# Performance work log

Measured on AMD Instinct MI355X. Metric: run time of the kernel, lower is better.

## Reference

```python
import jax, jax.numpy as jnp
import numpy as np

D_M, D_K, D_V, HEADS = 1024, 64, 64, 16
B, S = 2, 2048


def setup_inputs() -> dict:
    key = jax.random.key(0)
    ks = jax.random.split(key, 5)
    x = jax.random.normal(ks[0], (B, S, D_M), dtype=jnp.float32)
    # per-head projection weights (original deep-copies one rand init per head;
    # we give each head independent weights, matching the per-head param structure)
    Wk = jax.random.uniform(ks[1], (HEADS, D_M, D_K), dtype=jnp.float32)
    Wq = jax.random.uniform(ks[2], (HEADS, D_M, D_K), dtype=jnp.float32)
    Wv = jax.random.uniform(ks[3], (HEADS, D_M, D_V), dtype=jnp.float32)
    Wo = jax.random.uniform(ks[4], (HEADS * D_V, D_M), dtype=jnp.float32)
    return {"x": x, "Wk": Wk, "Wq": Wq, "Wv": Wv, "Wo": Wo}


def reference(x, Wk, Wq, Wv, Wo):
    # per-head QKV projections, batched over heads: [B,H,S,d]
    q = jnp.einsum("bsm,hmk->bhsk", x, Wq)
    k = jnp.einsum("bsm,hmk->bhsk", x, Wk)
    v = jnp.einsum("bsm,hmv->bhsv", x, Wv)
    scale = 1.0 / jnp.sqrt(jnp.asarray(q.shape[-1], dtype=q.dtype))
    scores = jnp.einsum("bhsk,bhtk->bhst", q, k) * scale  # [B,H,S,S]
    attn = jax.nn.softmax(scores, axis=-1)
    ctx = jnp.einsum("bhst,bhtv->bhsv", attn, v)  # [B,H,S,d_v]
    # concat heads -> [B,S,H*d_v], then output projection
    ctx = jnp.transpose(ctx, (0, 2, 1, 3)).reshape(x.shape[0], x.shape[1], -1)
    return jnp.einsum("bsc,cm->bsm", ctx, Wo)
```

## Files before the change

### kernel.cpp

```cpp
#include <hip/hip_runtime.h>
#include <hip/hip_bf16.h>
#include <stdint.h>

#define DM   1024
#define DKV  64
#define HEADS 16
#define BATCH 2
#define SEQ  2048
#define BS   (BATCH*SEQ)
#define BHD  (BATCH*HEADS)

typedef __attribute__((ext_vector_type(8))) short bf16x8;
typedef __attribute__((ext_vector_type(4))) short bf16x4;
typedef __attribute__((ext_vector_type(4))) float f32x4;

__device__ inline unsigned fb(float f) { union { float f; unsigned u; } v; v.f = f; return v.u; }

__device__ inline unsigned short bf16_rtn(float f) {
  unsigned u = fb(f);
  unsigned r = u + 0x7fffu + ((u >> 16) & 1u);
  return (unsigned short)(r >> 16);
}
__device__ inline float bf16_to_f(unsigned short h) {
  union { unsigned u; float f; } v; v.u = ((unsigned)h) << 16; return v.f;
}
__device__ inline void split_bf16(float x, unsigned short& hi, unsigned short& lo) {
  hi = bf16_rtn(x);
  lo = bf16_rtn(x - bf16_to_f(hi));
}
__device__ inline unsigned pack2_bf16(float lo_elem, float hi_elem) {
  return __builtin_amdgcn_perm(fb(hi_elem) + 0x8000u, fb(lo_elem) + 0x8000u, 0x07060302u);
}

__device__ inline float fast_exp2(float x) {
#if __has_builtin(__builtin_amdgcn_exp2f)
  return __builtin_amdgcn_exp2f(x);
#else
  return exp2f(x);
#endif
}

__device__ inline float max3f(float a, float b, float c) {
  return fmaxf(fmaxf(a, b), c);
}

__device__ inline f32x4 mfma16x16x16_bf16(bf16x4 a, bf16x4 b, f32x4 c) {
#if __has_builtin(__builtin_amdgcn_mfma_f32_16x16x16bf16_1k)
  return __builtin_amdgcn_mfma_f32_16x16x16bf16_1k(a, b, c, 0, 0, 0);
#else
  asm volatile("v_mfma_f32_16x16x16_bf16 %0, %1, %2, %0" : "+v"(c) : "v"(a), "v"(b));
  return c;
#endif
}

__device__ inline void stage16(const unsigned short* g, unsigned short* lds_base, int lane) {
#if __has_builtin(__builtin_amdgcn_global_load_lds)
  __builtin_amdgcn_global_load_lds((__attribute__((address_space(1))) void*)(g),
                                   (__attribute__((address_space(3))) void*)(lds_base),
                                   16, 0, 0);
#else
  *(bf16x8*)(lds_base + lane * 8) = *(const bf16x8*)g;
#endif
}

__device__ inline int swz(int row, int chunk) {
  return row * 64 + (((chunk ^ (row & 7)) & 7) << 3);
}

__global__ void prep(const float* __restrict__ x,
                     const float* __restrict__ Wq, const float* __restrict__ Wk,
                     const float* __restrict__ Wv, const float* __restrict__ Wo,
                     unsigned short* __restrict__ xh, unsigned short* __restrict__ xl,
                     unsigned short* __restrict__ Wh, unsigned short* __restrict__ Wl,
                     unsigned short* __restrict__ WoT) {
  __shared__ float tile[64][65];
  const int bid = blockIdx.x;
  const int t = threadIdx.x;

  if (bid < 2048) {
    int i = (bid * 256 + t) * 8;
    bf16x8 oh, ol;
    #pragma unroll
    for (int j = 0; j < 8; ++j) {
      unsigned short hi, lo;
      split_bf16(x[i + j], hi, lo);
      oh[j] = (short)hi; ol[j] = (short)lo;
    }
    *(bf16x8*)(xh + i) = oh;
    *(bf16x8*)(xl + i) = ol;
    return;
  }
  if (bid < 2816) {
    int b2 = bid - 2048;
    int p = b2 >> 8, h = (b2 >> 4) & 15, mt = b2 & 15;
    const float* W = (p == 0) ? Wq : (p == 1) ? Wk : Wv;
    const float* src = W + (size_t)h * (DM * DKV);
    int m0 = mt * 64;
    #pragma unroll
    for (int pass = 0; pass < 16; ++pass) {
      int row = pass * 4 + (t >> 6), col = t & 63;
      tile[row][col] = src[(size_t)(m0 + row) * DKV + col];
    }
    __syncthreads();
    int cbase = p * 1024 + h * 64;
    #pragma unroll
    for (int pass = 0; pass < 16; ++pass) {
      int krow = pass * 4 + (t >> 6), mcol = t & 63;
      unsigned short hi, lo;
      split_bf16(tile[mcol][krow], hi, lo);
      size_t idx = (size_t)(cbase + krow) * DM + m0 + mcol;
      Wh[idx] = hi; Wl[idx] = lo;
    }
    return;
  }
  {
    int b3 = bid - 2816;
    int ib = b3 >> 4, jb = b3 & 15;
    #pragma unroll
    for (int pass = 0; pass < 16; ++pass) {
      int row = pass * 4 + (t >> 6), col = t & 63;
      tile[row][col] = Wo[(size_t)(ib * 64 + row) * DM + jb * 64 + col];
    }
    __syncthreads();
    #pragma unroll
    for (int pass = 0; pass < 16; ++pass) {
      int a = pass * 4 + (t >> 6), b = t & 63;
      WoT[(size_t)(jb * 64 + a) * DM + ib * 64 + b] = bf16_rtn(tile[b][a]);
    }
  }
}

__global__ __launch_bounds__(256, 2)
void gemm_qkv(const unsigned short* __restrict__ Ah, const unsigned short* __restrict__ Al,
              const unsigned short* __restrict__ Bh, const unsigned short* __restrict__ Bl,
              unsigned short* __restrict__ Qh, unsigned short* __restrict__ Ql,
              unsigned short* __restrict__ Kh, unsigned short* __restrict__ Kl,
              unsigned short* __restrict__ Vt) {
  __shared__ unsigned short smem[32768];
  const int tid = threadIdx.x;
  const int w = tid >> 6, lane = tid & 63;
  const int quad = lane >> 4, l16 = lane & 15;
  const int wm = w >> 1, wn = w & 1;
  const int bid = blockIdx.x;
  const int r8 = lane >> 3, c8 = lane & 7;
  const int cs = c8 ^ r8;

  if (bid < 512) {
    unsigned short* AsH = smem;
    unsigned short* AsL = smem + 8192;
    unsigned short* BsH = smem + 16384;
    unsigned short* BsL = smem + 24576;
    const int bn = bid & 15, bm = bid >> 4;

    f32x4 acc[4][4];
    #pragma unroll
    for (int i = 0; i < 4; ++i)
      #pragma unroll
      for (int j = 0; j < 4; ++j) acc[i][j] = (f32x4){0.f, 0.f, 0.f, 0.f};

    const size_t offA = (size_t)(bm * 128 + w * 32 + r8) * DM + cs * 8;
    const size_t offB = (size_t)(bn * 128 + w * 32 + r8) * DM + cs * 8;

    for (int kk = 0; kk < DM / 64; ++kk) {
      #pragma unroll
      for (int ps = 0; ps < 4; ++ps) {
        stage16(Ah + offA + kk * 64 + ps * 8 * DM, AsH + (w * 32 + ps * 8) * 64, lane);
        stage16(Al + offA + kk * 64 + ps * 8 * DM, AsL + (w * 32 + ps * 8) * 64, lane);
        stage16(Bh + offB + kk * 64 + ps * 8 * DM, BsH + (w * 32 + ps * 8) * 64, lane);
        stage16(Bl + offB + kk * 64 + ps * 8 * DM, BsL + (w * 32 + ps * 8) * 64, lane);
      }
      asm volatile("s_waitcnt vmcnt(0)" ::: "memory");
      __syncthreads();
      #pragma unroll
      for (int ks = 0; ks < 2; ++ks) {
        bf16x8 afh[4], afl[4], bfh[4], bfl[4];
        #pragma unroll
        for (int mt = 0; mt < 4; ++mt) {
          int row = wm * 64 + mt * 16 + l16;
          int ad = row * 64 + ((((ks * 4 + quad) ^ (row & 7)) & 7) << 3);
          afh[mt] = *(const bf16x8*)(AsH + ad);
          afl[mt] = *(const bf16x8*)(AsL + ad);
        }
        #pragma unroll
        for (int nt = 0; nt < 4; ++nt) {
          int row = wn * 64 + nt * 16 + l16;
          int ad = row * 64 + ((((ks * 4 + quad) ^ (row & 7)) & 7) << 3);
          bfh[nt] = *(const bf16x8*)(BsH + ad);
          bfl[nt] = *(const bf16x8*)(BsL + ad);
        }
        #pragma unroll
        for (int mt = 0; mt < 4; ++mt)
          #pragma unroll
          for (int nt = 0; nt < 4; ++nt) {
            acc[mt][nt] = __builtin_amdgcn_mfma_f32_16x16x32_bf16(afh[mt], bfh[nt], acc[mt][nt], 0, 0, 0);
            acc[mt][nt] = __builtin_amdgcn_mfma_f32_16x16x32_bf16(afh[mt], bfl[nt], acc[mt][nt], 0, 0, 0);
            acc[mt][nt] = __builtin_amdgcn_mfma_f32_16x16x32_bf16(afl[mt], bfh[nt], acc[mt][nt], 0, 0, 0);
          }
      }
      __syncthreads();
    }

    const float SCL = 0.18033688011112042f;
    #pragma unroll
    for (int mt = 0; mt < 4; ++mt) {
      int m_g = bm * 128 + wm * 64 + mt * 16 + quad * 4;
      #pragma unroll
      for (int nt = 0; nt < 4; ++nt) {
        int n_g = bn * 128 + wn * 64 + nt * 16 + l16;
        int p = n_g >> 10, h = (n_g >> 6) & 15, k = n_g & 63;
        #pragma unroll
        for (int r = 0; r < 4; ++r) {
          int row = m_g + r;
          int b = row >> 11, s = row & 2047;
          int bh = b * HEADS + h;
          float v = acc[mt][nt][r];
          size_t idx = ((size_t)(bh * SEQ + s)) * DKV + k;
          unsigned short hi, lo;
          if (p == 0) {
            split_bf16(v * SCL, hi, lo);
            Qh[idx] = hi; Ql[idx] = lo;
          } else {
            split_bf16(v, hi, lo);
            Kh[idx] = hi; Kl[idx] = lo;
          }
        }
      }
    }
  } else {
    unsigned short* As = smem;
    unsigned short* Bs = smem + 4096;
    const int vid = bid - 512;
    const int bn = vid & 7, bm = vid >> 3;
    const unsigned short* Bt = Bh + (size_t)2048 * DM;

    f32x4 acc[2][4];
    #pragma unroll
    for (int i = 0; i < 2; ++i)
      #pragma unroll
      for (int j = 0; j < 4; ++j) acc[i][j] = (f32x4){0.f, 0.f, 0.f, 0.f};

    const size_t offA = (size_t)(bm * 64 + w * 16 + r8) * DM + cs * 8;
    const size_t offB = (size_t)(bn * 128 + w * 32 + r8) * DM + cs * 8;

    for (int kk = 0; kk < DM / 64; ++kk) {
      #pragma unroll
      for (int ps = 0; ps < 2; ++ps)
        stage16(Ah + offA + kk * 64 + ps * 8 * DM, As + (w * 16 + ps * 8) * 64, lane);
      #pragma unroll
      for (int ps = 0; ps < 4; ++ps)
        stage16(Bt + offB + kk * 64 + ps * 8 * DM, Bs + (w * 32 + ps * 8) * 64, lane);
      asm volatile("s_waitcnt vmcnt(0)" ::: "memory");
      __syncthreads();
      #pragma unroll
      for (int ks = 0; ks < 2; ++ks) {
        bf16x8 af[2], bfr[4];
        #pragma unroll
        for (int mt = 0; mt < 2; ++mt) {
          int row = wm * 32 + mt * 16 + l16;
          af[mt] = *(const bf16x8*)(As + row * 64 + ((((ks * 4 + quad) ^ (row & 7)) & 7) << 3));
        }
        #pragma unroll
        for (int nt = 0; nt < 4; ++nt) {
          int row = wn * 64 + nt * 16 + l16;
          bfr[nt] = *(const bf16x8*)(Bs + row * 64 + ((((ks * 4 + quad) ^ (row & 7)) & 7) << 3));
        }
        #pragma unroll
        for (int mt = 0; mt < 2; ++mt)
          #pragma unroll
          for (int nt = 0; nt < 4; ++nt)
            acc[mt][nt] = __builtin_amdgcn_mfma_f32_16x16x32_bf16(af[mt], bfr[nt], acc[mt][nt], 0, 0, 0);
      }
      __syncthreads();
    }

    #pragma unroll
    for (int mt = 0; mt < 2; ++mt) {
      int m_g = bm * 64 + wm * 32 + mt * 16 + quad * 4;
      #pragma unroll
      for (int nt = 0; nt < 4; ++nt) {
        int n_g = bn * 128 + wn * 64 + nt * 16 + l16;
        int h = n_g >> 6, k = n_g & 63;
        #pragma unroll
        for (int r = 0; r < 4; ++r) {
          int row = m_g + r;
          int b = row >> 11, s = row & 2047;
          int bh = b * HEADS + h;
          Vt[((size_t)(bh * DKV + k)) * SEQ + s] = bf16_rtn(acc[mt][nt][r]);
        }
      }
    }
  }
}

__global__ __launch_bounds__(256, 2)
void flash(const unsigned short* __restrict__ Qh, const unsigned short* __restrict__ Ql,
           const unsigned short* __restrict__ Kh, const unsigned short* __restrict__ Kl,
           const unsigned short* __restrict__ Vt, unsigned short* __restrict__ ctx) {
  __shared__ unsigned short KtH[2][64 * 64], KtL[2][64 * 64], Vts[2][64 * 64];
  const int tid = threadIdx.x;
  const int w = tid >> 6, lane = tid & 63, quad = lane >> 4, l16 = lane & 15;
  const int bh = blockIdx.x;
  const int q0 = blockIdx.y * 128;

  bf16x8 qfh[2][2], qfl[2][2];
  #pragma unroll
  for (int qt = 0; qt < 2; ++qt) {
    int qrow = q0 + w * 32 + qt * 16 + l16;
    size_t base = ((size_t)(bh * SEQ + qrow)) * DKV + quad * 8;
    qfh[qt][0] = *(const bf16x8*)(Qh + base);
    qfh[qt][1] = *(const bf16x8*)(Qh + base + 32);
    qfl[qt][0] = *(const bf16x8*)(Ql + base);
    qfl[qt][1] = *(const bf16x8*)(Ql + base + 32);
  }

  float m_run[2] = {-1e30f, -1e30f};
  float l_run[2] = {0.f, 0.f};
  f32x4 acc[2][4];
  #pragma unroll
  for (int qt = 0; qt < 2; ++qt)
    #pragma unroll
    for (int vt = 0; vt < 4; ++vt) acc[qt][vt] = (f32x4){0.f, 0.f, 0.f, 0.f};

  const int srow = w * 16 + (lane >> 3);
  const int csrc = (lane & 7) ^ (lane >> 3);
  const unsigned short* kh_src = Kh + ((size_t)(bh * SEQ) + srow) * DKV + csrc * 8;
  const unsigned short* kl_src = Kl + ((size_t)(bh * SEQ) + srow) * DKV + csrc * 8;
  const unsigned short* v_src  = Vt + ((size_t)(bh * DKV) + srow) * SEQ + csrc * 8;

  #define STAGE_K(buf, kt0)                                                     \
    do {                                                                        \
      unsigned short* dH = &KtH[buf][(w * 16) * 64];                            \
      unsigned short* dL = &KtL[buf][(w * 16) * 64];                            \
      stage16(kh_src + (size_t)(kt0) * 64 * DKV,           dH,       lane);     \
      stage16(kh_src + (size_t)(kt0) * 64 * DKV + 8 * DKV, dH + 512, lane);     \
      stage16(kl_src + (size_t)(kt0) * 64 * DKV,           dL,       lane);     \
      stage16(kl_src + (size_t)(kt0) * 64 * DKV + 8 * DKV, dL + 512, lane);     \
    } while (0)
  #define STAGE_V(buf, kt0)                                                     \
    do {                                                                        \
      unsigned short* dV = &Vts[buf][(w * 16) * 64];                            \
      stage16(v_src + (kt0) * 64,           dV,       lane);                    \
      stage16(v_src + (kt0) * 64 + 8 * SEQ, dV + 512, lane);                    \
    } while (0)

  #define QK_HALF(STV, KHP, KLP, MT0)                                           \
    _Pragma("unroll")                                                           \
    for (int mt = (MT0); mt < (MT0) + 2; ++mt) {                                \
      int rowA = mt * 16 + l16;                                                 \
      bf16x8 kah0 = *(const bf16x8*)((KHP) + swz(rowA, quad));                  \
      bf16x8 kah1 = *(const bf16x8*)((KHP) + swz(rowA, quad + 4));              \
      bf16x8 kal0 = *(const bf16x8*)((KLP) + swz(rowA, quad));                  \
      bf16x8 kal1 = *(const bf16x8*)((KLP) + swz(rowA, quad + 4));              \
      _Pragma("unroll")                                                         \
      for (int qt = 0; qt < 2; ++qt) {                                          \
        f32x4 c = (f32x4){0.f, 0.f, 0.f, 0.f};                                  \
        c = __builtin_amdgcn_mfma_f32_16x16x32_bf16(kah0, qfh[qt][0], c, 0, 0, 0); \
        c = __builtin_amdgcn_mfma_f32_16x16x32_bf16(kah1, qfh[qt][1], c, 0, 0, 0); \
        c = __builtin_amdgcn_mfma_f32_16x16x32_bf16(kah0, qfl[qt][0], c, 0, 0, 0); \
        c = __builtin_amdgcn_mfma_f32_16x16x32_bf16(kah1, qfl[qt][1], c, 0, 0, 0); \
        c = __builtin_amdgcn_mfma_f32_16x16x32_bf16(kal0, qfh[qt][0], c, 0, 0, 0); \
        c = __builtin_amdgcn_mfma_f32_16x16x32_bf16(kal1, qfh[qt][1], c, 0, 0, 0); \
        (STV)[mt][qt] = c;                                                      \
      }                                                                         \
    }

  #define SM_QT(QT)                                                             \
    {                                                                           \
      float x0 = max3f(st[0][QT][0], st[0][QT][1], st[0][QT][2]);               \
      float x1 = max3f(st[0][QT][3], st[1][QT][0], st[1][QT][1]);               \
      float x2 = max3f(st[1][QT][2], st[1][QT][3], st[2][QT][0]);               \
      float x3 = max3f(st[2][QT][1], st[2][QT][2], st[2][QT][3]);               \
      float x4 = max3f(st[3][QT][0], st[3][QT][1], st[3][QT][2]);               \
      float cm = fmaxf(max3f(x0, x1, x2), max3f(x3, x4, st[3][QT][3]));         \
      if (!__all(cm <= m_run[QT] + 8.0f)) {                                     \
        cm = fmaxf(cm, __shfl_xor(cm, 16));                                     \
        cm = fmaxf(cm, __shfl_xor(cm, 32));                                     \
        float mn = fmaxf(cm, m_run[QT]);                                        \
        float alpha = fast_exp2(m_run[QT] - mn);                                \
        m_run[QT] = mn;                                                         \
        l_run[QT] *= alpha;                                                     \
        _Pragma("unroll")                                                       \
        for (int vt = 0; vt < 4; ++vt) acc[QT][vt] = acc[QT][vt] * alpha;       \
      }                                                                         \
      float mn = m_run[QT];                                                     \
      float ssum = 0.f;                                                         \
      _Pragma("unroll")                                                         \
      for (int mt = 0; mt < 4; ++mt) {                                          \
        float p0 = fast_exp2(st[mt][QT][0] - mn);                               \
        float p1 = fast_exp2(st[mt][QT][1] - mn);                               \
        float p2 = fast_exp2(st[mt][QT][2] - mn);                               \
        float p3 = fast_exp2(st[mt][QT][3] - mn);                               \
        ssum += (p0 + p1) + (p2 + p3);                                          \
        union { bf16x4 v; unsigned u2[2]; } pk;                                 \
        pk.u2[0] = pack2_bf16(p0, p1);                                          \
        pk.u2[1] = pack2_bf16(p2, p3);                                          \
        pb[QT][mt] = pk.v;                                                      \
      }                                                                         \
      l_run[QT] += ssum;                                                        \
    }

  #define PV_ALL(VSP)                                                           \
    _Pragma("unroll")                                                           \
    for (int vt = 0; vt < 4; ++vt)                                              \
      _Pragma("unroll")                                                         \
      for (int mt = 0; mt < 4; ++mt) {                                          \
        int row = vt * 16 + l16;                                                \
        int addr = row * 64 + ((((mt * 2 + (quad >> 1)) ^ (row & 7)) & 7) << 3) + (quad & 1) * 4; \
        bf16x4 va = *(const bf16x4*)((VSP) + addr);                             \
        _Pragma("unroll")                                                       \
        for (int qt = 0; qt < 2; ++qt)                                          \
          acc[qt][vt] = mfma16x16x16_bf16(va, pb[qt][mt], acc[qt][vt]);         \
      }

  STAGE_K(0, 0);
  STAGE_V(0, 0);
  STAGE_K(1, 1);
  asm volatile("s_waitcnt vmcnt(0)" ::: "memory");
  __syncthreads();

  f32x4 st[4][2];
  __builtin_amdgcn_s_setprio(1);
  QK_HALF(st, KtH[0], KtL[0], 0);
  QK_HALF(st, KtH[0], KtL[0], 2);
  __builtin_amdgcn_s_setprio(0);

  #pragma unroll 2
  for (int t = 0; t < SEQ / 64 - 1; ++t) {
    const int cb = t & 1, nb = (t + 1) & 1;
    if (t + 2 < SEQ / 64) STAGE_K(cb, t + 2);
    STAGE_V(nb, t + 1);

    const unsigned short* kHn = KtH[nb];
    const unsigned short* kLn = KtL[nb];
    const unsigned short* vS  = Vts[cb];

    bf16x4 pb[2][4];
    f32x4 stn[4][2];
    SM_QT(0);
    __builtin_amdgcn_s_setprio(1);
    QK_HALF(stn, kHn, kLn, 0);
    __builtin_amdgcn_s_setprio(0);
    SM_QT(1);
    __builtin_amdgcn_s_setprio(1);
    QK_HALF(stn, kHn, kLn, 2);
    PV_ALL(vS);
    __builtin_amdgcn_s_setprio(0);

    #pragma unroll
    for (int mt = 0; mt < 4; ++mt)
      #pragma unroll
      for (int qt = 0; qt < 2; ++qt) st[mt][qt] = stn[mt][qt];

    asm volatile("s_waitcnt vmcnt(0)" ::: "memory");
    __syncthreads();
  }

  {
    bf16x4 pb[2][4];
    SM_QT(0);
    SM_QT(1);
    PV_ALL(Vts[(SEQ / 64 - 1) & 1]);
  }
  #undef STAGE_K
  #undef STAGE_V
  #undef QK_HALF
  #undef SM_QT
  #undef PV_ALL

  int h = bh & 15, b = bh >> 4;
  #pragma unroll
  for (int qt = 0; qt < 2; ++qt) {
    float lt = l_run[qt];
    lt += __shfl_xor(lt, 16);
    lt += __shfl_xor(lt, 32);
    float inv = 1.0f / lt;
    int bs = b * SEQ + q0 + w * 32 + qt * 16 + l16;
    #pragma unroll
    for (int vt = 0; vt < 4; ++vt) {
      union { bf16x4 v; unsigned u2[2]; } pk;
      pk.u2[0] = pack2_bf16(acc[qt][vt][0] * inv, acc[qt][vt][1] * inv);
      pk.u2[1] = pack2_bf16(acc[qt][vt][2] * inv, acc[qt][vt][3] * inv);
      *(bf16x4*)(ctx + (size_t)bs * DM + h * 64 + vt * 16 + quad * 4) = pk.v;
    }
  }
}

__global__ __launch_bounds__(256, 2)
void gemm_out(const unsigned short* __restrict__ A, const unsigned short* __restrict__ Bt,
              float* __restrict__ out) {
  __shared__ unsigned short As[64 * 64];
  __shared__ unsigned short Bs[128 * 64];
  const int tid = threadIdx.x;
  const int w = tid >> 6, lane = tid & 63;
  const int quad = lane >> 4, l16 = lane & 15;
  const int wm = w >> 1, wn = w & 1;
  const int bn = blockIdx.x, bm = blockIdx.y;

  f32x4 acc[2][4];
  #pragma unroll
  for (int i = 0; i < 2; ++i)
    #pragma unroll
    for (int j = 0; j < 4; ++j) acc[i][j] = (f32x4){0.f, 0.f, 0.f, 0.f};

  const int r8 = lane >> 3, c8 = lane & 7;
  const int cs = c8 ^ r8;
  const size_t offA = (size_t)(bm * 64 + w * 16 + r8) * DM + cs * 8;
  const size_t offB = (size_t)(bn * 128 + w * 32 + r8) * DM + cs * 8;

  for (int kk = 0; kk < DM / 64; ++kk) {
    #pragma unroll
    for (int ps = 0; ps < 2; ++ps)
      stage16(A + offA + kk * 64 + ps * 8 * DM, As + (w * 16 + ps * 8) * 64, lane);
    #pragma unroll
    for (int ps = 0; ps < 4; ++ps)
      stage16(Bt + offB + kk * 64 + ps * 8 * DM, Bs + (w * 32 + ps * 8) * 64, lane);
    asm volatile("s_waitcnt vmcnt(0)" ::: "memory");
    __syncthreads();
    #pragma unroll
    for (int ks = 0; ks < 2; ++ks) {
      bf16x8 af[2], bfr[4];
      #pragma unroll
      for (int mt = 0; mt < 2; ++mt) {
        int row = wm * 32 + mt * 16 + l16;
        af[mt] = *(const bf16x8*)(As + row * 64 + ((((ks * 4 + quad) ^ (row & 7)) & 7) << 3));
      }
      #pragma unroll
      for (int nt = 0; nt < 4; ++nt) {
        int row = wn * 64 + nt * 16 + l16;
        bfr[nt] = *(const bf16x8*)(Bs + row * 64 + ((((ks * 4 + quad) ^ (row & 7)) & 7) << 3));
      }
      #pragma unroll
      for (int mt = 0; mt < 2; ++mt)
        #pragma unroll
        for (int nt = 0; nt < 4; ++nt)
          acc[mt][nt] = __builtin_amdgcn_mfma_f32_16x16x32_bf16(af[mt], bfr[nt], acc[mt][nt], 0, 0, 0);
    }
    __syncthreads();
  }

  #pragma unroll
  for (int mt = 0; mt < 2; ++mt) {
    int m_g = bm * 64 + wm * 32 + mt * 16 + quad * 4;
    #pragma unroll
    for (int nt = 0; nt < 4; ++nt) {
      int n_g = bn * 128 + wn * 64 + nt * 16 + l16;
      #pragma unroll
      for (int r = 0; r < 4; ++r)
        out[(size_t)(m_g + r) * DM + n_g] = acc[mt][nt][r];
    }
  }
}

extern "C" void kernel_launch(void* const* d_in, const int* in_sizes, int n_in,
                              void* d_out, int out_size, void* d_ws, size_t ws_size,
                              hipStream_t stream) {
  const float* x  = (const float*)d_in[0];
  const float* Wk = (const float*)d_in[1];
  const float* Wq = (const float*)d_in[2];
  const float* Wv = (const float*)d_in[3];
  const float* Wo = (const float*)d_in[4];
  float* out = (float*)d_out;

  unsigned short* xh  = (unsigned short*)d_ws;
  unsigned short* xl  = xh  + (size_t)BS * DM;
  unsigned short* Wh  = xl  + (size_t)BS * DM;
  unsigned short* Wl  = Wh  + (size_t)3 * DM * DM;
  unsigned short* WoT = Wl  + (size_t)3 * DM * DM;
  unsigned short* Qh  = WoT + (size_t)DM * DM;
  unsigned short* Ql  = Qh  + (size_t)BHD * SEQ * DKV;
  unsigned short* Kh  = Ql  + (size_t)BHD * SEQ * DKV;
  unsigned short* Kl  = Kh  + (size_t)BHD * SEQ * DKV;
  unsigned short* Vtb = Kl  + (size_t)BHD * SEQ * DKV;
  unsigned short* ctx = Vtb + (size_t)BHD * SEQ * DKV;

  prep<<<3072, 256, 0, stream>>>(x, Wq, Wk, Wv, Wo, xh, xl, Wh, Wl, WoT);
  gemm_qkv<<<1024, 256, 0, stream>>>(xh, xl, Wh, Wl, Qh, Ql, Kh, Kl, Vtb);
  flash<<<dim3(BHD, SEQ / 128), 256, 0, stream>>>(Qh, Ql, Kh, Kl, Vtb, ctx);
  gemm_out<<<dim3(8, 64), 256, 0, stream>>>(ctx, WoT, out);
}
```

Measured before the change: 235.0 us.

## Triple-buffer K tiles in flash attention and relax the per-iteration vmcnt wait

```diff
diff --git a/kernel.cpp b/kernel.cpp
--- a/kernel.cpp
+++ b/kernel.cpp
@@ -38,10 +38,6 @@
 #else
   return exp2f(x);
 #endif
-}
-
-__device__ inline float max3f(float a, float b, float c) {
-  return fmaxf(fmaxf(a, b), c);
 }
 
 __device__ inline f32x4 mfma16x16x16_bf16(bf16x4 a, bf16x4 b, f32x4 c) {
@@ -296,11 +292,12 @@
 void flash(const unsigned short* __restrict__ Qh, const unsigned short* __restrict__ Ql,
            const unsigned short* __restrict__ Kh, const unsigned short* __restrict__ Kl,
            const unsigned short* __restrict__ Vt, unsigned short* __restrict__ ctx) {
-  __shared__ unsigned short KtH[2][64 * 64], KtL[2][64 * 64], Vts[2][64 * 64];
+  __shared__ unsigned short KtH[3][64 * 64], KtL[3][64 * 64], Vts[2][64 * 64];
   const int tid = threadIdx.x;
   const int w = tid >> 6, lane = tid & 63, quad = lane >> 4, l16 = lane & 15;
   const int bh = blockIdx.x;
   const int q0 = blockIdx.y * 128;
+  const int NT = SEQ / 64;
 
   bf16x8 qfh[2][2], qfl[2][2];
   #pragma unroll
@@ -366,12 +363,11 @@
 
   #define SM_QT(QT)                                                             \
     {                                                                           \
-      float x0 = max3f(st[0][QT][0], st[0][QT][1], st[0][QT][2]);               \
-      float x1 = max3f(st[0][QT][3], st[1][QT][0], st[1][QT][1]);               \
-      float x2 = max3f(st[1][QT][2], st[1][QT][3], st[2][QT][0]);               \
-      float x3 = max3f(st[2][QT][1], st[2][QT][2], st[2][QT][3]);               \
-      float x4 = max3f(st[3][QT][0], st[3][QT][1], st[3][QT][2]);               \
-      float cm = fmaxf(max3f(x0, x1, x2), max3f(x3, x4, st[3][QT][3]));         \
+      float cm = -1e30f;                                                        \
+      _Pragma("unroll")                                                         \
+      for (int mt = 0; mt < 4; ++mt)                                            \
+        _Pragma("unroll")                                                       \
+        for (int r = 0; r < 4; ++r) cm = fmaxf(cm, st[mt][QT][r]);              \
       if (!__all(cm <= m_run[QT] + 8.0f)) {                                     \
         cm = fmaxf(cm, __shfl_xor(cm, 16));                                     \
         cm = fmaxf(cm, __shfl_xor(cm, 32));                                     \
@@ -415,24 +411,28 @@
   STAGE_K(0, 0);
   STAGE_V(0, 0);
   STAGE_K(1, 1);
-  asm volatile("s_waitcnt vmcnt(0)" ::: "memory");
-  __syncthreads();
+  STAGE_K(2, 2);
+  asm volatile("s_waitcnt vmcnt(4)" ::: "memory");
+  __builtin_amdgcn_s_barrier();
+  __builtin_amdgcn_sched_barrier(0);
 
   f32x4 st[4][2];
   __builtin_amdgcn_s_setprio(1);
   QK_HALF(st, KtH[0], KtL[0], 0);
   QK_HALF(st, KtH[0], KtL[0], 2);
   __builtin_amdgcn_s_setprio(0);
+  __builtin_amdgcn_s_barrier();
+  __builtin_amdgcn_sched_barrier(0);
 
   #pragma unroll 2
-  for (int t = 0; t < SEQ / 64 - 1; ++t) {
-    const int cb = t & 1, nb = (t + 1) & 1;
-    if (t + 2 < SEQ / 64) STAGE_K(cb, t + 2);
-    STAGE_V(nb, t + 1);
-
-    const unsigned short* kHn = KtH[nb];
-    const unsigned short* kLn = KtL[nb];
-    const unsigned short* vS  = Vts[cb];
+  for (int t = 0; t < NT - 1; ++t) {
+    STAGE_V((t + 1) & 1, t + 1);
+    if (t + 3 < NT) STAGE_K(t % 3, t + 3);
+
+    const int kslot = (t + 1) % 3;
+    const unsigned short* kHn = KtH[kslot];
+    const unsigned short* kLn = KtL[kslot];
+    const unsigned short* vS  = Vts[t & 1];
 
     bf16x4 pb[2][4];
     f32x4 stn[4][2];
@@ -451,15 +451,20 @@
       #pragma unroll
       for (int qt = 0; qt < 2; ++qt) st[mt][qt] = stn[mt][qt];
 
-    asm volatile("s_waitcnt vmcnt(0)" ::: "memory");
-    __syncthreads();
+    if (t < NT - 3) {
+      asm volatile("s_waitcnt vmcnt(4)" ::: "memory");
+    } else {
+      asm volatile("s_waitcnt vmcnt(0)" ::: "memory");
+    }
+    __builtin_amdgcn_s_barrier();
+    __builtin_amdgcn_sched_barrier(0);
   }
 
   {
     bf16x4 pb[2][4];
     SM_QT(0);
     SM_QT(1);
-    PV_ALL(Vts[(SEQ / 64 - 1) & 1]);
+    PV_ALL(Vts[(NT - 1) & 1]);
   }
   #undef STAGE_K
   #undef STAGE_V
```

Result: slower. 244.4 us (+4.0%).
